# Kernel tuning notes

Measured on AMD Instinct MI355X. Metric: run time of the kernel, lower is better.

The kernel has to match this reference:

```python
import jax, jax.numpy as jnp
import numpy as np

NUM_HEADS = 12


def _rel_lookup(rel_pos, size):
    # q_size == k_size == size, table length == 2*size-1: pure gather, no interp
    idx = jnp.arange(size)[:, None] - jnp.arange(size)[None, :] + (size - 1)
    return rel_pos[idx]  # (size, size, head_dim)


def setup_inputs() -> dict:
    key = jax.random.key(0)
    ks = jax.random.split(key, 7)
    B, H, W, C = 8, 32, 32, 768
    return {
        "x": jax.random.normal(ks[0], (B, H, W, C), dtype=jnp.float32),
        "w_qkv": jax.random.normal(ks[1], (C, 3 * C), dtype=jnp.float32) * 0.02,
        "b_qkv": jax.random.normal(ks[2], (3 * C,), dtype=jnp.float32) * 0.02,
        "w_proj": jax.random.normal(ks[3], (C, C), dtype=jnp.float32) * 0.02,
        "b_proj": jax.random.normal(ks[4], (C,), dtype=jnp.float32) * 0.02,
        "rel_pos_h": jax.random.normal(ks[5], (2 * H - 1, C // NUM_HEADS), dtype=jnp.float32) * 0.02,
        "rel_pos_w": jax.random.normal(ks[6], (2 * W - 1, C // NUM_HEADS), dtype=jnp.float32) * 0.02,
    }


def reference(x, w_qkv, b_qkv, w_proj, b_proj, rel_pos_h, rel_pos_w):
    B, H, W, C = x.shape
    nh = NUM_HEADS
    hd = C // nh
    scale = hd ** -0.5

    qkv = x @ w_qkv + b_qkv  # (B,H,W,3C)
    qkv = qkv.reshape(B, H * W, 3, nh, hd).transpose(2, 0, 3, 1, 4)
    qkv = qkv.reshape(3, B * nh, H * W, hd)
    q, k, v = qkv[0], qkv[1], qkv[2]  # each (B*nh, HW, hd)

    attn = jnp.einsum('bqd,bkd->bqk', q * scale, k)  # (B*nh, HW, HW)

    Rh = _rel_lookup(rel_pos_h, H)  # (H,H,hd)
    Rw = _rel_lookup(rel_pos_w, W)  # (W,W,hd)
    r_q = q.reshape(B * nh, H, W, hd)
    rel_h = jnp.einsum('bhwc,hkc->bhwk', r_q, Rh)  # (B*nh,H,W,H)
    rel_w = jnp.einsum('bhwc,wkc->bhwk', r_q, Rw)  # (B*nh,H,W,W)
    attn = (attn.reshape(B * nh, H, W, H, W)
            + rel_h[:, :, :, :, None]
            + rel_w[:, :, :, None, :]).reshape(B * nh, H * W, H * W)

    attn = jax.nn.softmax(attn, axis=-1)
    out = jnp.einsum('bqk,bkd->bqd', attn, v)  # (B*nh, HW, hd)
    out = out.reshape(B, nh, H, W, hd).transpose(0, 2, 3, 1, 4).reshape(B, H, W, C)
    return out @ w_proj + b_proj
```

## Files before the change

kernel.cpp:

```cpp
#include <hip/hip_runtime.h>

typedef unsigned short u16;
typedef unsigned int u32;
typedef __attribute__((ext_vector_type(8))) short short8;
typedef __attribute__((ext_vector_type(4))) float f32x4;
typedef __attribute__((ext_vector_type(4))) u32 u32x4;

__device__ __forceinline__ u16 f2bf(float f) {
  u32 u = __float_as_uint(f);
  return (u16)((u + 0x7FFFu + ((u >> 16) & 1u)) >> 16);
}
__device__ __forceinline__ float bf2f(u16 u) { return __uint_as_float(((u32)u) << 16); }
__device__ __forceinline__ f32x4 zero4() { f32x4 z = {0.f, 0.f, 0.f, 0.f}; return z; }

__device__ __forceinline__ u32 cvt_pk_bf16(float lo, float hi) {
  u32 r;
  asm("v_cvt_pk_bf16_f32 %0, %1, %2" : "=v"(r) : "v"(lo), "v"(hi));
  return r;
}

__device__ __forceinline__ void g2lds16(const void* g, void* l) {
  __builtin_amdgcn_global_load_lds((const __attribute__((address_space(1))) void*)g,
                                   (__attribute__((address_space(3))) void*)l, 16, 0, 0);
}

#define LOG2E 1.44269504088896340736f

__global__ __launch_bounds__(256) void cvt_x_kernel(const float* __restrict__ in,
                                                    u16* __restrict__ out, int n4) {
  int i = blockIdx.x * 256 + threadIdx.x;
  if (i >= n4) return;
  float4 v = ((const float4*)in)[i];
  ushort4 o;
  o.x = f2bf(v.x); o.y = f2bf(v.y); o.z = f2bf(v.z); o.w = f2bf(v.w);
  ((ushort4*)out)[i] = o;
}

__global__ __launch_bounds__(256) void transp_cvt_kernel(const float* __restrict__ in,
                                                         u16* __restrict__ out, int K, int N) {
  __shared__ float t[32][33];
  int n0 = blockIdx.x * 32, k0 = blockIdx.y * 32;
  int tx = threadIdx.x & 31, ty = threadIdx.x >> 5;
#pragma unroll
  for (int r = 0; r < 4; ++r)
    t[ty + r * 8][tx] = in[(size_t)(k0 + ty + r * 8) * N + n0 + tx];
  __syncthreads();
#pragma unroll
  for (int r = 0; r < 4; ++r)
    out[(size_t)(n0 + ty + r * 8) * K + k0 + tx] = f2bf(t[tx][ty + r * 8]);
}

template <int EPI>
__global__ __launch_bounds__(256, 3) void gemm_bt_kernel(
    const u16* __restrict__ A, const u16* __restrict__ Bt, const float* __restrict__ bias,
    int M, int N, int K,
    u16* __restrict__ q_out, u16* __restrict__ k_out, u16* __restrict__ vT_out,
    float* __restrict__ f_out) {
  __shared__ __align__(16) u16 As[128 * 64];
  __shared__ __align__(16) u16 Bs[128 * 64];
  const int tid = threadIdx.x;
  const int w = tid >> 6, lane = tid & 63;

  const int nwg = gridDim.x * gridDim.y;
  const int flat = blockIdx.y * gridDim.x + blockIdx.x;
  const int wg = (flat & 7) * (nwg >> 3) + (flat >> 3);
  const int bx = wg % gridDim.x, by = wg / gridDim.x;
  const int m0 = by * 128, n0 = bx * 128;
  const int wm0 = (w >> 1) * 64, wn0 = (w & 1) * 64;

  f32x4 acc[4][4];
#pragma unroll
  for (int i = 0; i < 4; ++i)
#pragma unroll
    for (int j = 0; j < 4; ++j) acc[i][j] = zero4();

  const int stgRow = lane >> 3;
  const int stgChunk = ((lane & 7) ^ (lane >> 3)) * 8;
  const int g = lane >> 4, lc = lane & 15;
  const int lr = g << 2;

  for (int kt = 0; kt < K; kt += 64) {
    __syncthreads();
#pragma unroll
    for (int jj = 0; jj < 4; ++jj) {
      int i = w + jj * 4;
      g2lds16(A + (size_t)(m0 + i * 8 + stgRow) * K + kt + stgChunk, (char*)As + i * 1024);
    }
#pragma unroll
    for (int jj = 0; jj < 4; ++jj) {
      int i = w + jj * 4;
      g2lds16(Bt + (size_t)(n0 + i * 8 + stgRow) * K + kt + stgChunk, (char*)Bs + i * 1024);
    }
    __syncthreads();
#pragma unroll
    for (int ks = 0; ks < 2; ++ks) {
      short8 af[4], bfr[4];
#pragma unroll
      for (int r = 0; r < 4; ++r) {
        int rowA = wm0 + r * 16 + lc;
        af[r] = *(const short8*)((const char*)As + rowA * 128 +
                                 ((((ks << 2) | g) ^ (lc & 7)) << 4));
        int rowB = wn0 + r * 16 + lc;
        bfr[r] = *(const short8*)((const char*)Bs + rowB * 128 +
                                  ((((ks << 2) | g) ^ (lc & 7)) << 4));
      }
      __builtin_amdgcn_s_setprio(1);
#pragma unroll
      for (int i = 0; i < 4; ++i)
#pragma unroll
        for (int j = 0; j < 4; ++j)
          acc[i][j] = __builtin_amdgcn_mfma_f32_16x16x32_bf16(af[i], bfr[j], acc[i][j], 0, 0, 0);
      __builtin_amdgcn_s_setprio(0);
    }
  }

#pragma unroll
  for (int j = 0; j < 4; ++j) {
    int n = n0 + wn0 + j * 16 + lc;
    float bv = bias[n];
    if (EPI == 0) {
      int three = n / 768;
      int rem = n - three * 768;
      int head = rem >> 6, d = rem & 63;
#pragma unroll
      for (int i = 0; i < 4; ++i) {
        if (three == 2) {
          int t0 = ((m0 + wm0 + i * 16 + lr) & 1023);
          int bb = (m0 + wm0 + i * 16 + lr) >> 10;
          size_t bh = (size_t)bb * 12 + head;
          ushort4 ov;
          ov.x = f2bf(acc[i][j][0] + bv);
          ov.y = f2bf(acc[i][j][1] + bv);
          ov.z = f2bf(acc[i][j][2] + bv);
          ov.w = f2bf(acc[i][j][3] + bv);
          *(ushort4*)(vT_out + (bh * 64 + d) * 1024 + t0) = ov;
        } else {
#pragma unroll
          for (int r = 0; r < 4; ++r) {
            int m = m0 + wm0 + i * 16 + lr + r;
            int bb = m >> 10, t = m & 1023;
            size_t bh = (size_t)bb * 12 + head;
            float val = acc[i][j][r] + bv;
            if (three == 0)
              q_out[(bh * 1024 + t) * 64 + d] = f2bf(val * (0.125f * LOG2E));
            else
              k_out[(bh * 1024 + t) * 64 + d] = f2bf(val);
          }
        }
      }
    } else {
#pragma unroll
      for (int i = 0; i < 4; ++i)
#pragma unroll
        for (int r = 0; r < 4; ++r) {
          int m = m0 + wm0 + i * 16 + lr + r;
          f_out[(size_t)m * N + n] = acc[i][j][r] + bv;
        }
    }
  }
}

__global__ __launch_bounds__(256) void rel_kernel(const u16* __restrict__ qs,
                                                  const float* __restrict__ rph,
                                                  const float* __restrict__ rpw,
                                                  float* __restrict__ relh,
                                                  float* __restrict__ relw) {
  __shared__ __align__(16) float Ts[63 * 68];
  __shared__ __align__(16) u16 Qs[32 * 72];
  const int tid = threadIdx.x;
  const int h = blockIdx.x, bh = blockIdx.y;
  const int mode = blockIdx.z;
  const float* table = mode ? rpw : rph;
  float* out = mode ? relw : relh;
  for (int i = tid; i < (63 * 64) / 4; i += 256) {
    float4 v = ((const float4*)table)[i];
    int row = i >> 4, col = (i & 15) * 4;
    *(float4*)(Ts + row * 68 + col) = v;
  }
  const u16* qrow = qs + ((size_t)bh * 1024 + h * 32) * 64;
  for (int i = tid; i < (32 * 64) / 8; i += 256) {
    uint4 v = ((const uint4*)qrow)[i];
    int row = i >> 3, col = (i & 7) * 8;
    *(uint4*)(Qs + row * 72 + col) = v;
  }
  __syncthreads();
  const int w = tid >> 3;
  const int kx = tid & 7;
  const int base = mode ? w : h;
  float acc0 = 0.f, acc1 = 0.f, acc2 = 0.f, acc3 = 0.f;
  const u16* qp = Qs + w * 72;
#pragma unroll
  for (int dc = 0; dc < 8; ++dc) {
    uint4 qv = *(const uint4*)(qp + dc * 8);
    float qf[8];
    qf[0] = bf2f((u16)(qv.x & 0xffff)); qf[1] = bf2f((u16)(qv.x >> 16));
    qf[2] = bf2f((u16)(qv.y & 0xffff)); qf[3] = bf2f((u16)(qv.y >> 16));
    qf[4] = bf2f((u16)(qv.z & 0xffff)); qf[5] = bf2f((u16)(qv.z >> 16));
    qf[6] = bf2f((u16)(qv.w & 0xffff)); qf[7] = bf2f((u16)(qv.w >> 16));
#pragma unroll
    for (int jj = 0; jj < 4; ++jj) {
      int row = base - (kx + 8 * jj) + 31;
      const float* tp = Ts + row * 68 + dc * 8;
      float4 p0 = ((const float4*)tp)[0];
      float4 p1 = ((const float4*)tp)[1];
      float s = qf[0] * p0.x + qf[1] * p0.y + qf[2] * p0.z + qf[3] * p0.w +
                qf[4] * p1.x + qf[5] * p1.y + qf[6] * p1.z + qf[7] * p1.w;
      if (jj == 0) acc0 += s;
      else if (jj == 1) acc1 += s;
      else if (jj == 2) acc2 += s;
      else acc3 += s;
    }
  }
  float* op = out + ((size_t)bh * 1024 + h * 32 + w) * 32 + kx;
  op[0] = acc0 * 8.f;
  op[8] = acc1 * 8.f;
  op[16] = acc2 * 8.f;
  op[24] = acc3 * 8.f;
}

__global__ __launch_bounds__(256) void flash_kernel(
    const u16* __restrict__ qs, const u16* __restrict__ kb, const u16* __restrict__ vT,
    const float* __restrict__ relh, const float* __restrict__ relw, u16* __restrict__ ao) {
  __shared__ __align__(16) u16 Ks[2 * 64 * 64];
  __shared__ __align__(16) u16 Vs[2 * 64 * 64];
  __shared__ __align__(16) float RhS[64 * 33];
  __shared__ __align__(16) u32 PpT[4][32 * 20];
  const int tid = threadIdx.x, wv = tid >> 6, lane = tid & 63;
  const int nwg = gridDim.x * gridDim.y;
  const int flat = blockIdx.y * gridDim.x + blockIdx.x;
  const int wg = (flat & 7) * (nwg >> 3) + (flat >> 3);
  const int qt = wg & 15, bh = wg >> 4;
  const int q0 = qt * 64;
  const int g = lane >> 4, lc = lane & 15;

  const float* rh_g = relh + ((size_t)bh * 1024 + q0) * 32;
  for (int i = tid; i < 64 * 32; i += 256) RhS[(i >> 5) * 33 + (i & 31)] = rh_g[i];

  const size_t qbase = ((size_t)bh * 1024 + q0 + wv * 16 + lc) * 64;
  short8 aq0 = *(const short8*)(qs + qbase + g * 8);
  short8 aq1 = *(const short8*)(qs + qbase + 32 + g * 8);

  const float* rwp = relw + ((size_t)bh * 1024 + q0 + wv * 16 + lc) * 32 + 4 * g;
  float4 rw0 = *(const float4*)(rwp);
  float4 rw1 = *(const float4*)(rwp + 16);
  float rwr[8] = {rw0.x, rw0.y, rw0.z, rw0.w, rw1.x, rw1.y, rw1.z, rw1.w};

  f32x4 o[4];
#pragma unroll
  for (int ct = 0; ct < 4; ++ct) o[ct] = zero4();
  float lsum = 0.f;
  const int rhbase = (wv * 16 + lc) * 33;

  const int stgRow = lane >> 3;
  const int stgChunk = ((lane & 7) ^ (lane >> 3)) * 8;
  u32* pt = &PpT[wv][0];

#define STAGE(buf, ktS)                                                                   \
  do {                                                                                    \
    const int k0s = (ktS) * 64;                                                           \
    _Pragma("unroll") for (int jj = 0; jj < 4; ++jj) {                                    \
      int i = wv + jj * 4;                                                                \
      if (i < 8)                                                                          \
        g2lds16(kb + ((size_t)bh * 1024 + k0s + i * 8 + stgRow) * 64 + stgChunk,          \
                (char*)Ks + (buf) * 8192 + i * 1024);                                     \
      else                                                                                \
        g2lds16(vT + ((size_t)bh * 64 + (i - 8) * 8 + stgRow) * 1024 + k0s + stgChunk,    \
                (char*)Vs + (buf) * 8192 + (i - 8) * 1024);                               \
    }                                                                                     \
  } while (0)

  STAGE(0, 0);
  __syncthreads();

  for (int kt = 0; kt < 16; ++kt) {
    const int cur = kt & 1;
    if (kt < 15) STAGE(cur ^ 1, kt + 1);

    f32x4 s[4];
    __builtin_amdgcn_s_setprio(1);
#pragma unroll
    for (int ct = 0; ct < 4; ++ct) {
      int key = ct * 16 + lc;
      int sw = (key & 7) << 4;
      const char* kp = (const char*)Ks + cur * 8192 + key * 128;
      short8 kf0 = *(const short8*)(kp + ((g * 16) ^ sw));
      short8 kf1 = *(const short8*)(kp + ((64 + g * 16) ^ sw));
      f32x4 z = zero4();
      z = __builtin_amdgcn_mfma_f32_16x16x32_bf16(kf0, aq0, z, 0, 0, 0);
      z = __builtin_amdgcn_mfma_f32_16x16x32_bf16(kf1, aq1, z, 0, 0, 0);
      s[ct] = z;
    }
    __builtin_amdgcn_s_setprio(0);

    float rh0 = RhS[rhbase + kt * 2 + 0];
    float rh1 = RhS[rhbase + kt * 2 + 1];
    float pr[4][4];
#pragma unroll
    for (int ct = 0; ct < 4; ++ct)
#pragma unroll
      for (int r = 0; r < 4; ++r)
        pr[ct][r] = __builtin_amdgcn_exp2f(s[ct][r] + (ct < 2 ? rh0 : rh1) +
                                           rwr[(ct & 1) * 4 + r]);

    lsum += ((pr[0][0] + pr[0][1]) + (pr[0][2] + pr[0][3])) +
            ((pr[1][0] + pr[1][1]) + (pr[1][2] + pr[1][3])) +
            ((pr[2][0] + pr[2][1]) + (pr[2][2] + pr[2][3])) +
            ((pr[3][0] + pr[3][1]) + (pr[3][2] + pr[3][3]));

#pragma unroll
    for (int ct = 0; ct < 4; ++ct) {
      u32 w0 = cvt_pk_bf16(pr[ct][0], pr[ct][1]);
      u32 w1 = cvt_pk_bf16(pr[ct][2], pr[ct][3]);
      pt[(8 * ct + 2 * g + 0) * 20 + lc] = w0;
      pt[(8 * ct + 2 * g + 1) * 20 + lc] = w1;
    }

    union { u32x4 u; short8 s; } pb0, pb1;
#pragma unroll
    for (int p = 0; p < 4; ++p) {
      pb0.u[p] = pt[(4 * g + p) * 20 + lc];
      pb1.u[p] = pt[(16 + 4 * g + p) * 20 + lc];
    }

    __builtin_amdgcn_s_setprio(1);
#pragma unroll
    for (int ct = 0; ct < 4; ++ct) {
      int d = ct * 16 + lc;
      int sw = (d & 7) << 4;
      const char* vp = (const char*)Vs + cur * 8192 + d * 128;
      short8 vf0 = *(const short8*)(vp + ((g * 16) ^ sw));
      short8 vf1 = *(const short8*)(vp + ((64 + g * 16) ^ sw));
      o[ct] = __builtin_amdgcn_mfma_f32_16x16x32_bf16(vf0, pb0.s, o[ct], 0, 0, 0);
      o[ct] = __builtin_amdgcn_mfma_f32_16x16x32_bf16(vf1, pb1.s, o[ct], 0, 0, 0);
    }
    __builtin_amdgcn_s_setprio(0);

    __syncthreads();
  }

  lsum += __shfl_xor(lsum, 16);
  lsum += __shfl_xor(lsum, 32);
  float inv = 1.0f / lsum;

  const int b_ = bh / 12, head = bh - b_ * 12;
  u16* op = ao + ((size_t)b_ * 1024 + q0 + wv * 16 + lc) * 768 + head * 64 + 4 * g;
#pragma unroll
  for (int ct = 0; ct < 4; ++ct) {
    ushort4 ov;
    ov.x = f2bf(o[ct][0] * inv);
    ov.y = f2bf(o[ct][1] * inv);
    ov.z = f2bf(o[ct][2] * inv);
    ov.w = f2bf(o[ct][3] * inv);
    *(ushort4*)(op + ct * 16) = ov;
  }
#undef STAGE
}

extern "C" void kernel_launch(void* const* d_in, const int* in_sizes, int n_in,
                              void* d_out, int out_size, void* d_ws, size_t ws_size,
                              hipStream_t stream) {
  const float* x = (const float*)d_in[0];
  const float* w_qkv = (const float*)d_in[1];
  const float* b_qkv = (const float*)d_in[2];
  const float* w_proj = (const float*)d_in[3];
  const float* b_proj = (const float*)d_in[4];
  const float* rph = (const float*)d_in[5];
  const float* rpw = (const float*)d_in[6];
  (void)in_sizes; (void)n_in; (void)out_size; (void)ws_size;

  char* ws = (char*)d_ws;
  size_t off = 0;
  auto alloc = [&](size_t bytes) {
    void* p = ws + off;
    off += (bytes + 255) & ~(size_t)255;
    return p;
  };
  u16* xb = (u16*)alloc((size_t)8192 * 768 * 2);
  float* relh = (float*)xb;
  u16* wqkvT = (u16*)alloc((size_t)2304 * 768 * 2);
  u16* wprojT = (u16*)alloc((size_t)768 * 768 * 2);
  u16* qsb = (u16*)alloc((size_t)96 * 1024 * 64 * 2);
  u16* kbb = (u16*)alloc((size_t)96 * 1024 * 64 * 2);
  u16* vTb = (u16*)alloc((size_t)96 * 64 * 1024 * 2);
  float* relw = (float*)alloc((size_t)96 * 1024 * 32 * 4);
  u16* ao = (u16*)alloc((size_t)8192 * 768 * 2);

  cvt_x_kernel<<<dim3(8192 * 768 / 4 / 256), 256, 0, stream>>>(x, xb, 8192 * 768 / 4);
  transp_cvt_kernel<<<dim3(2304 / 32, 768 / 32), 256, 0, stream>>>(w_qkv, wqkvT, 768, 2304);
  transp_cvt_kernel<<<dim3(768 / 32, 768 / 32), 256, 0, stream>>>(w_proj, wprojT, 768, 768);
  gemm_bt_kernel<0><<<dim3(2304 / 128, 8192 / 128), 256, 0, stream>>>(
      xb, wqkvT, b_qkv, 8192, 2304, 768, qsb, kbb, vTb, nullptr);
  rel_kernel<<<dim3(32, 96, 2), 256, 0, stream>>>(qsb, rph, rpw, relh, relw);
  flash_kernel<<<dim3(16, 96), 256, 0, stream>>>(qsb, kbb, vTb, relh, relw, ao);
  gemm_bt_kernel<1><<<dim3(768 / 128, 8192 / 128), 256, 0, stream>>>(
      ao, wprojT, b_proj, 8192, 768, 768, nullptr, nullptr, nullptr, (float*)d_out);
}
```

Measured before the change: 150.5 us.

## Process two query tiles per flash block and read V directly from global

The flash attention kernel now handles 128 queries per workgroup as two 64-row sub-tiles. Each K tile staged in LDS is reused for twice as many score MFMAs, and the grid is halved. V is no longer staged through LDS. Each wave loads its V^T fragments straight from global memory, and a launch-bounds occupancy hint is added. The aim is to halve K/V traffic per query and cut LDS staging. The cost is higher register pressure and uncoalesced, non-prefetched V loads sitting on the critical path before the PV MFMAs.

New measurement: 162.4 us. +7.9%, slower.

```diff
diff --git a/kernel.cpp b/kernel.cpp
--- a/kernel.cpp
+++ b/kernel.cpp
@@ -218,65 +218,67 @@
   op[24] = acc3 * 8.f;
 }
 
-__global__ __launch_bounds__(256) void flash_kernel(
+__global__ __launch_bounds__(256, 3) void flash_kernel(
     const u16* __restrict__ qs, const u16* __restrict__ kb, const u16* __restrict__ vT,
     const float* __restrict__ relh, const float* __restrict__ relw, u16* __restrict__ ao) {
   __shared__ __align__(16) u16 Ks[2 * 64 * 64];
-  __shared__ __align__(16) u16 Vs[2 * 64 * 64];
-  __shared__ __align__(16) float RhS[64 * 33];
+  __shared__ __align__(16) float RhS[128 * 33];
   __shared__ __align__(16) u32 PpT[4][32 * 20];
   const int tid = threadIdx.x, wv = tid >> 6, lane = tid & 63;
   const int nwg = gridDim.x * gridDim.y;
   const int flat = blockIdx.y * gridDim.x + blockIdx.x;
   const int wg = (flat & 7) * (nwg >> 3) + (flat >> 3);
-  const int qt = wg & 15, bh = wg >> 4;
-  const int q0 = qt * 64;
+  const int qt = wg & 7, bh = wg >> 3;
+  const int q0 = qt * 128;
   const int g = lane >> 4, lc = lane & 15;
 
   const float* rh_g = relh + ((size_t)bh * 1024 + q0) * 32;
-  for (int i = tid; i < 64 * 32; i += 256) RhS[(i >> 5) * 33 + (i & 31)] = rh_g[i];
-
-  const size_t qbase = ((size_t)bh * 1024 + q0 + wv * 16 + lc) * 64;
-  short8 aq0 = *(const short8*)(qs + qbase + g * 8);
-  short8 aq1 = *(const short8*)(qs + qbase + 32 + g * 8);
-
-  const float* rwp = relw + ((size_t)bh * 1024 + q0 + wv * 16 + lc) * 32 + 4 * g;
-  float4 rw0 = *(const float4*)(rwp);
-  float4 rw1 = *(const float4*)(rwp + 16);
-  float rwr[8] = {rw0.x, rw0.y, rw0.z, rw0.w, rw1.x, rw1.y, rw1.z, rw1.w};
-
-  f32x4 o[4];
-#pragma unroll
-  for (int ct = 0; ct < 4; ++ct) o[ct] = zero4();
-  float lsum = 0.f;
-  const int rhbase = (wv * 16 + lc) * 33;
+  for (int i = tid; i < 128 * 32; i += 256) RhS[(i >> 5) * 33 + (i & 31)] = rh_g[i];
+
+  const size_t qbaseA = ((size_t)bh * 1024 + q0 + wv * 16 + lc) * 64;
+  const size_t qbaseB = qbaseA + (size_t)64 * 64;
+  short8 aq0 = *(const short8*)(qs + qbaseA + g * 8);
+  short8 aq1 = *(const short8*)(qs + qbaseA + 32 + g * 8);
+  short8 aq2 = *(const short8*)(qs + qbaseB + g * 8);
+  short8 aq3 = *(const short8*)(qs + qbaseB + 32 + g * 8);
+
+  const float* rwpA = relw + ((size_t)bh * 1024 + q0 + wv * 16 + lc) * 32 + 4 * g;
+  const float* rwpB = rwpA + (size_t)64 * 32;
+  float4 ra0 = *(const float4*)(rwpA), ra1 = *(const float4*)(rwpA + 16);
+  float4 rb0 = *(const float4*)(rwpB), rb1 = *(const float4*)(rwpB + 16);
+  float rwrA[8] = {ra0.x, ra0.y, ra0.z, ra0.w, ra1.x, ra1.y, ra1.z, ra1.w};
+  float rwrB[8] = {rb0.x, rb0.y, rb0.z, rb0.w, rb1.x, rb1.y, rb1.z, rb1.w};
+
+  f32x4 o[4], o2[4];
+#pragma unroll
+  for (int ct = 0; ct < 4; ++ct) { o[ct] = zero4(); o2[ct] = zero4(); }
+  float lsumA = 0.f, lsumB = 0.f;
+  const int rhbaseA = (wv * 16 + lc) * 33;
+  const int rhbaseB = (64 + wv * 16 + lc) * 33;
 
   const int stgRow = lane >> 3;
   const int stgChunk = ((lane & 7) ^ (lane >> 3)) * 8;
   u32* pt = &PpT[wv][0];
 
-#define STAGE(buf, ktS)                                                                   \
+#define STAGEK(buf, ktS)                                                                  \
   do {                                                                                    \
     const int k0s = (ktS) * 64;                                                           \
-    _Pragma("unroll") for (int jj = 0; jj < 4; ++jj) {                                    \
-      int i = wv + jj * 4;                                                                \
-      if (i < 8)                                                                          \
-        g2lds16(kb + ((size_t)bh * 1024 + k0s + i * 8 + stgRow) * 64 + stgChunk,          \
-                (char*)Ks + (buf) * 8192 + i * 1024);                                     \
-      else                                                                                \
-        g2lds16(vT + ((size_t)bh * 64 + (i - 8) * 8 + stgRow) * 1024 + k0s + stgChunk,    \
-                (char*)Vs + (buf) * 8192 + (i - 8) * 1024);                               \
+    _Pragma("unroll") for (int jj = 0; jj < 2; ++jj) {                                    \
+      int i = wv + jj * 4;                                                      \
+      g2lds16(kb + ((size_t)bh * 1024 + k0s + i * 8 + stgRow) * 64 + stgChunk,            \
+              (char*)Ks + (buf) * 8192 + i * 1024);                                       \
     }                                                                                     \
   } while (0)
 
-  STAGE(0, 0);
+  STAGEK(0, 0);
   __syncthreads();
 
   for (int kt = 0; kt < 16; ++kt) {
     const int cur = kt & 1;
-    if (kt < 15) STAGE(cur ^ 1, kt + 1);
-
-    f32x4 s[4];
+    const int k0 = kt * 64;
+    if (kt < 15) STAGEK(cur ^ 1, kt + 1);
+
+    f32x4 sA[4], sB[4];
     __builtin_amdgcn_s_setprio(1);
 #pragma unroll
     for (int ct = 0; ct < 4; ++ct) {
@@ -285,75 +287,96 @@
       const char* kp = (const char*)Ks + cur * 8192 + key * 128;
       short8 kf0 = *(const short8*)(kp + ((g * 16) ^ sw));
       short8 kf1 = *(const short8*)(kp + ((64 + g * 16) ^ sw));
-      f32x4 z = zero4();
-      z = __builtin_amdgcn_mfma_f32_16x16x32_bf16(kf0, aq0, z, 0, 0, 0);
-      z = __builtin_amdgcn_mfma_f32_16x16x32_bf16(kf1, aq1, z, 0, 0, 0);
-      s[ct] = z;
+      f32x4 zA = zero4(), zB = zero4();
+      zA = __builtin_amdgcn_mfma_f32_16x16x32_bf16(kf0, aq0, zA, 0, 0, 0);
+      zA = __builtin_amdgcn_mfma_f32_16x16x32_bf16(kf1, aq1, zA, 0, 0, 0);
+      zB = __builtin_amdgcn_mfma_f32_16x16x32_bf16(kf0, aq2, zB, 0, 0, 0);
+      zB = __builtin_amdgcn_mfma_f32_16x16x32_bf16(kf1, aq3, zB, 0, 0, 0);
+      sA[ct] = zA;
+      sB[ct] = zB;
     }
     __builtin_amdgcn_s_setprio(0);
 
-    float rh0 = RhS[rhbase + kt * 2 + 0];
-    float rh1 = RhS[rhbase + kt * 2 + 1];
-    float pr[4][4];
+    float rh0A = RhS[rhbaseA + kt * 2 + 0], rh1A = RhS[rhbaseA + kt * 2 + 1];
+    float rh0B = RhS[rhbaseB + kt * 2 + 0], rh1B = RhS[rhbaseB + kt * 2 + 1];
+    float prA[4][4], prB[4][4];
 #pragma unroll
     for (int ct = 0; ct < 4; ++ct)
 #pragma unroll
-      for (int r = 0; r < 4; ++r)
-        pr[ct][r] = __builtin_amdgcn_exp2f(s[ct][r] + (ct < 2 ? rh0 : rh1) +
-                                           rwr[(ct & 1) * 4 + r]);
-
-    lsum += ((pr[0][0] + pr[0][1]) + (pr[0][2] + pr[0][3])) +
-            ((pr[1][0] + pr[1][1]) + (pr[1][2] + pr[1][3])) +
-            ((pr[2][0] + pr[2][1]) + (pr[2][2] + pr[2][3])) +
-            ((pr[3][0] + pr[3][1]) + (pr[3][2] + pr[3][3]));
-
+      for (int r = 0; r < 4; ++r) {
+        prA[ct][r] = __builtin_amdgcn_exp2f(sA[ct][r] + (ct < 2 ? rh0A : rh1A) +
+                                            rwrA[(ct & 1) * 4 + r]);
+        prB[ct][r] = __builtin_amdgcn_exp2f(sB[ct][r] + (ct < 2 ? rh0B : rh1B) +
+                                            rwrB[(ct & 1) * 4 + r]);
+      }
+    lsumA += ((prA[0][0] + prA[0][1]) + (prA[0][2] + prA[0][3])) +
+             ((prA[1][0] + prA[1][1]) + (prA[1][2] + prA[1][3])) +
+             ((prA[2][0] + prA[2][1]) + (prA[2][2] + prA[2][3])) +
+             ((prA[3][0] + prA[3][1]) + (prA[3][2] + prA[3][3]));
+    lsumB += ((prB[0][0] + prB[0][1]) + (prB[0][2] + prB[0][3])) +
+             ((prB[1][0] + prB[1][1]) + (prB[1][2] + prB[1][3])) +
+             ((prB[2][0] + prB[2][1]) + (prB[2][2] + prB[2][3])) +
+             ((prB[3][0] + prB[3][1]) + (prB[3][2] + prB[3][3]));
+
+    union { u32x4 u; short8 s; } pbA0, pbA1, pbB0, pbB1;
 #pragma unroll
     for (int ct = 0; ct < 4; ++ct) {
-      u32 w0 = cvt_pk_bf16(pr[ct][0], pr[ct][1]);
-      u32 w1 = cvt_pk_bf16(pr[ct][2], pr[ct][3]);
-      pt[(8 * ct + 2 * g + 0) * 20 + lc] = w0;
-      pt[(8 * ct + 2 * g + 1) * 20 + lc] = w1;
-    }
-
-    union { u32x4 u; short8 s; } pb0, pb1;
+      pt[(8 * ct + 2 * g + 0) * 20 + lc] = cvt_pk_bf16(prA[ct][0], prA[ct][1]);
+      pt[(8 * ct + 2 * g + 1) * 20 + lc] = cvt_pk_bf16(prA[ct][2], prA[ct][3]);
+    }
 #pragma unroll
     for (int p = 0; p < 4; ++p) {
-      pb0.u[p] = pt[(4 * g + p) * 20 + lc];
-      pb1.u[p] = pt[(16 + 4 * g + p) * 20 + lc];
+      pbA0.u[p] = pt[(4 * g + p) * 20 + lc];
+      pbA1.u[p] = pt[(16 + 4 * g + p) * 20 + lc];
+    }
+#pragma unroll
+    for (int ct = 0; ct < 4; ++ct) {
+      pt[(8 * ct + 2 * g + 0) * 20 + lc] = cvt_pk_bf16(prB[ct][0], prB[ct][1]);
+      pt[(8 * ct + 2 * g + 1) * 20 + lc] = cvt_pk_bf16(prB[ct][2], prB[ct][3]);
+    }
+#pragma unroll
+    for (int p = 0; p < 4; ++p) {
+      pbB0.u[p] = pt[(4 * g + p) * 20 + lc];
+      pbB1.u[p] = pt[(16 + 4 * g + p) * 20 + lc];
     }
 
     __builtin_amdgcn_s_setprio(1);
 #pragma unroll
     for (int ct = 0; ct < 4; ++ct) {
       int d = ct * 16 + lc;
-      int sw = (d & 7) << 4;
-      const char* vp = (const char*)Vs + cur * 8192 + d * 128;
-      short8 vf0 = *(const short8*)(vp + ((g * 16) ^ sw));
-      short8 vf1 = *(const short8*)(vp + ((64 + g * 16) ^ sw));
-      o[ct] = __builtin_amdgcn_mfma_f32_16x16x32_bf16(vf0, pb0.s, o[ct], 0, 0, 0);
-      o[ct] = __builtin_amdgcn_mfma_f32_16x16x32_bf16(vf1, pb1.s, o[ct], 0, 0, 0);
+      const u16* vp = vT + ((size_t)bh * 64 + d) * 1024 + k0 + 8 * g;
+      short8 vf0 = *(const short8*)(vp);
+      short8 vf1 = *(const short8*)(vp + 32);
+      o[ct] = __builtin_amdgcn_mfma_f32_16x16x32_bf16(vf0, pbA0.s, o[ct], 0, 0, 0);
+      o[ct] = __builtin_amdgcn_mfma_f32_16x16x32_bf16(vf1, pbA1.s, o[ct], 0, 0, 0);
+      o2[ct] = __builtin_amdgcn_mfma_f32_16x16x32_bf16(vf0, pbB0.s, o2[ct], 0, 0, 0);
+      o2[ct] = __builtin_amdgcn_mfma_f32_16x16x32_bf16(vf1, pbB1.s, o2[ct], 0, 0, 0);
     }
     __builtin_amdgcn_s_setprio(0);
 
     __syncthreads();
   }
 
-  lsum += __shfl_xor(lsum, 16);
-  lsum += __shfl_xor(lsum, 32);
-  float inv = 1.0f / lsum;
+  lsumA += __shfl_xor(lsumA, 16);
+  lsumA += __shfl_xor(lsumA, 32);
+  lsumB += __shfl_xor(lsumB, 16);
+  lsumB += __shfl_xor(lsumB, 32);
+  float invA = 1.0f / lsumA, invB = 1.0f / lsumB;
 
   const int b_ = bh / 12, head = bh - b_ * 12;
-  u16* op = ao + ((size_t)b_ * 1024 + q0 + wv * 16 + lc) * 768 + head * 64 + 4 * g;
+  u16* opA = ao + ((size_t)b_ * 1024 + q0 + wv * 16 + lc) * 768 + head * 64 + 4 * g;
+  u16* opB = opA + (size_t)64 * 768;
 #pragma unroll
   for (int ct = 0; ct < 4; ++ct) {
-    ushort4 ov;
-    ov.x = f2bf(o[ct][0] * inv);
-    ov.y = f2bf(o[ct][1] * inv);
-    ov.z = f2bf(o[ct][2] * inv);
-    ov.w = f2bf(o[ct][3] * inv);
-    *(ushort4*)(op + ct * 16) = ov;
-  }
-#undef STAGE
+    ushort4 ovA, ovB;
+    ovA.x = f2bf(o[ct][0] * invA); ovA.y = f2bf(o[ct][1] * invA);
+    ovA.z = f2bf(o[ct][2] * invA); ovA.w = f2bf(o[ct][3] * invA);
+    ovB.x = f2bf(o2[ct][0] * invB); ovB.y = f2bf(o2[ct][1] * invB);
+    ovB.z = f2bf(o2[ct][2] * invB); ovB.w = f2bf(o2[ct][3] * invB);
+    *(ushort4*)(opA + ct * 16) = ovA;
+    *(ushort4*)(opB + ct * 16) = ovB;
+  }
+#undef STAGEK
 }
 
 extern "C" void kernel_launch(void* const* d_in, const int* in_sizes, int n_in,
@@ -391,7 +414,7 @@
   gemm_bt_kernel<0><<<dim3(2304 / 128, 8192 / 128), 256, 0, stream>>>(
       xb, wqkvT, b_qkv, 8192, 2304, 768, qsb, kbb, vTb, nullptr);
   rel_kernel<<<dim3(32, 96, 2), 256, 0, stream>>>(qsb, rph, rpw, relh, relw);
-  flash_kernel<<<dim3(16, 96), 256, 0, stream>>>(qsb, kbb, vTb, relh, relw, ao);
+  flash_kernel<<<dim3(8, 96), 256, 0, stream>>>(qsb, kbb, vTb, relh, relw, ao);
   gemm_bt_kernel<1><<<dim3(768 / 128, 8192 / 128), 256, 0, stream>>>(
       ao, wprojT, b_proj, 8192, 768, 768, nullptr, nullptr, nullptr, (float*)d_out);
 }
```

## Double-buffer GEMM LDS tiles with BK=32 to overlap global loads

Applied to the files above, without the earlier changes.

Restructures the bf16 GEMM main loop from single-buffered 64-wide K tiles to two 32-wide K buffers, prefetching the next tile via direct global-to-LDS loads while MFMAs run on the current one. The XOR swizzle is redone for 64-byte rows, and the loop now uses one barrier per iteration instead of two. The aim is to hide global load latency behind compute. In exchange there are twice as many loop iterations, with smaller per-iteration MFMA work and more barrier overhead.

Result: slower. 158.0 us (+5.0%).

```diff
diff --git a/kernel.cpp b/kernel.cpp
--- a/kernel.cpp
+++ b/kernel.cpp
@@ -56,8 +56,8 @@
     int M, int N, int K,
     u16* __restrict__ q_out, u16* __restrict__ k_out, u16* __restrict__ vT_out,
     float* __restrict__ f_out) {
-  __shared__ __align__(16) u16 As[128 * 64];
-  __shared__ __align__(16) u16 Bs[128 * 64];
+  __shared__ __align__(16) u16 As[2 * 128 * 32];
+  __shared__ __align__(16) u16 Bs[2 * 128 * 32];
   const int tid = threadIdx.x;
   const int w = tid >> 6, lane = tid & 63;
 
@@ -74,45 +74,48 @@
 #pragma unroll
     for (int j = 0; j < 4; ++j) acc[i][j] = zero4();
 
-  const int stgRow = lane >> 3;
-  const int stgChunk = ((lane & 7) ^ (lane >> 3)) * 8;
+  const int sRow = lane >> 2;
+  const int sChunk = ((lane & 3) ^ ((lane >> 3) & 3)) * 8;
+  const int cw = ((lane >> 4) << 4) ^ (((lane >> 1) & 3) << 4);
   const int g = lane >> 4, lc = lane & 15;
   const int lr = g << 2;
 
-  for (int kt = 0; kt < K; kt += 64) {
+#define GSTAGE(buf, ktS)                                                                   \
+  do {                                                                                     \
+    _Pragma("unroll") for (int jj = 0; jj < 4; ++jj) {                                     \
+      int i = w + jj * 4;                                                                  \
+      if (i < 8)                                                                           \
+        g2lds16(A + (size_t)(m0 + i * 16 + sRow) * K + (ktS) + sChunk,                     \
+                (char*)As + (buf) * 8192 + i * 1024);                                      \
+      else                                                                                 \
+        g2lds16(Bt + (size_t)(n0 + (i - 8) * 16 + sRow) * K + (ktS) + sChunk,              \
+                (char*)Bs + (buf) * 8192 + (i - 8) * 1024);                                \
+    }                                                                                      \
+  } while (0)
+
+  const int nk = K >> 5;
+  GSTAGE(0, 0);
+  __syncthreads();
+
+  for (int kti = 0; kti < nk; ++kti) {
+    const int cur = kti & 1;
+    if (kti + 1 < nk) GSTAGE(cur ^ 1, (kti + 1) << 5);
+    short8 af[4], bfr[4];
+#pragma unroll
+    for (int r = 0; r < 4; ++r) {
+      af[r] = *(const short8*)((const char*)As + cur * 8192 + (wm0 + r * 16 + lc) * 64 + cw);
+      bfr[r] = *(const short8*)((const char*)Bs + cur * 8192 + (wn0 + r * 16 + lc) * 64 + cw);
+    }
+    __builtin_amdgcn_s_setprio(1);
+#pragma unroll
+    for (int i = 0; i < 4; ++i)
+#pragma unroll
+      for (int j = 0; j < 4; ++j)
+        acc[i][j] = __builtin_amdgcn_mfma_f32_16x16x32_bf16(af[i], bfr[j], acc[i][j], 0, 0, 0);
+    __builtin_amdgcn_s_setprio(0);
     __syncthreads();
-#pragma unroll
-    for (int jj = 0; jj < 4; ++jj) {
-      int i = w + jj * 4;
-      g2lds16(A + (size_t)(m0 + i * 8 + stgRow) * K + kt + stgChunk, (char*)As + i * 1024);
-    }
-#pragma unroll
-    for (int jj = 0; jj < 4; ++jj) {
-      int i = w + jj * 4;
-      g2lds16(Bt + (size_t)(n0 + i * 8 + stgRow) * K + kt + stgChunk, (char*)Bs + i * 1024);
-    }
-    __syncthreads();
-#pragma unroll
-    for (int ks = 0; ks < 2; ++ks) {
-      short8 af[4], bfr[4];
-#pragma unroll
-      for (int r = 0; r < 4; ++r) {
-        int rowA = wm0 + r * 16 + lc;
-        af[r] = *(const short8*)((const char*)As + rowA * 128 +
-                                 ((((ks << 2) | g) ^ (lc & 7)) << 4));
-        int rowB = wn0 + r * 16 + lc;
-        bfr[r] = *(const short8*)((const char*)Bs + rowB * 128 +
-                                  ((((ks << 2) | g) ^ (lc & 7)) << 4));
-      }
-      __builtin_amdgcn_s_setprio(1);
-#pragma unroll
-      for (int i = 0; i < 4; ++i)
-#pragma unroll
-        for (int j = 0; j < 4; ++j)
-          acc[i][j] = __builtin_amdgcn_mfma_f32_16x16x32_bf16(af[i], bfr[j], acc[i][j], 0, 0, 0);
-      __builtin_amdgcn_s_setprio(0);
-    }
-  }
+  }
+#undef GSTAGE
 
 #pragma unroll
   for (int j = 0; j < 4; ++j) {
```
